# Performance work log

Hardware: AMD Instinct MI355X
Metric: run time of the kernel (lower is better)

Reference implementation:

```python
import jax, jax.numpy as jnp
import numpy as np

EPS = 1e-5

def setup_inputs() -> dict:
    key = jax.random.key(0)
    ks = jax.random.split(key, 16)
    n_users, n_items, d = 100000, 50000, 128
    n_nodes = n_users + n_items
    E = 4800000
    B = 16384
    h1, h2 = 256, 128
    xavier = lambda k, shp: jax.random.uniform(k, shp, jnp.float32, -1.0, 1.0) * np.sqrt(6.0 / (shp[0] + shp[1]))
    inp = {
        'user_indices': jax.random.randint(ks[0], (B,), 0, n_users),
        'item_indices': jax.random.randint(ks[1], (B,), 0, n_items),
        'edge_rows': jax.random.randint(ks[2], (E,), 0, n_nodes, dtype=jnp.int32),
        'edge_cols': jax.random.randint(ks[3], (E,), 0, n_nodes, dtype=jnp.int32),
        'edge_vals': jax.random.uniform(ks[4], (E,), jnp.float32),
        'user_emb': xavier(ks[5], (n_users, d)),
        'item_emb': xavier(ks[6], (n_items, d)),
        'W1': xavier(ks[7], (d, h1)), 'b1': jnp.zeros((h1,), jnp.float32),
        'g1': jnp.ones((h1,), jnp.float32), 'beta1': jnp.zeros((h1,), jnp.float32),
        'W2': xavier(ks[8], (h1, h2)), 'b2': jnp.zeros((h2,), jnp.float32),
        'g2': jnp.ones((h2,), jnp.float32), 'beta2': jnp.zeros((h2,), jnp.float32),
        'P1': xavier(ks[9], (2 * h2, h2)), 'pb1': jnp.zeros((h2,), jnp.float32),
        'P2': xavier(ks[10], (h2, 1)), 'pb2': jnp.zeros((1,), jnp.float32),
    }
    return inp

def _gcn_layer(x, rows, cols, vals, n_nodes, W, b, g, beta):
    # linear transform then sparse adjacency aggregation (COO):
    # out[r] = sum_{e: rows[e]==r} vals[e] * t[cols[e]]
    t = x @ W + b                                   # [N, out]
    agg = jax.ops.segment_sum(vals[:, None] * t[cols], rows, num_segments=n_nodes)
    # BatchNorm1d (training-mode batch statistics over nodes)
    mu = jnp.mean(agg, axis=0)
    var = jnp.var(agg, axis=0)
    out = (agg - mu) * jax.lax.rsqrt(var + EPS) * g + beta
    return jax.nn.relu(out)                         # dropout = identity (eval)

def reference(user_indices, item_indices, edge_rows, edge_cols, edge_vals,
              user_emb, item_emb, W1, b1, g1, beta1, W2, b2, g2, beta2,
              P1, pb1, P2, pb2):
    n_users = user_emb.shape[0]
    x = jnp.concatenate([user_emb, item_emb], axis=0)  # [N, d]
    n_nodes = x.shape[0]
    x = _gcn_layer(x, edge_rows, edge_cols, edge_vals, n_nodes, W1, b1, g1, beta1)
    x = _gcn_layer(x, edge_rows, edge_cols, edge_vals, n_nodes, W2, b2, g2, beta2)
    u = x[:n_users][user_indices]                      # [B, h2]
    v = x[n_users:][item_indices]                      # [B, h2]
    combined = jnp.concatenate([u, v], axis=-1)        # [B, 2*h2]
    h = jax.nn.relu(combined @ P1 + pb1)
    pred = (h @ P2 + pb2).squeeze(-1)                  # [B]
    return pred
```

## Files before the change

### kernel.cpp

```cpp
#include <hip/hip_runtime.h>
#include <stdint.h>

#define N_USERS 100000
#define N_NODES 150000
#define D0      128
#define H1      256
#define H2      128
#define NEDGE   4800000
#define BATCH   16384
#define EPSV    1e-5f
#define NBUCK   147
#define BCHUNK  4096
#define CCHUNK  16384

typedef short short8  __attribute__((ext_vector_type(8)));
typedef float floatx4 __attribute__((ext_vector_type(4)));
typedef unsigned short u16;

__device__ inline float bf2f(u16 u) {
    union { float f; uint32_t i; } x; x.i = ((uint32_t)u) << 16; return x.f;
}
__device__ inline u16 f2bf(float f) {
    union { float f; uint32_t i; } x; x.f = f;
    return (u16)((x.i + 0x7FFFu + ((x.i >> 16) & 1u)) >> 16);
}
__device__ inline float itof(uint32_t u) {
    union { float f; uint32_t i; } x; x.i = u; return x.f;
}
__device__ inline uint32_t ftoi(float f) {
    union { float f; uint32_t i; } x; x.f = f; return x.i;
}
__device__ inline uint32_t pack2(float a, float b) {
    return (uint32_t)f2bf(a) | ((uint32_t)f2bf(b) << 16);
}

__global__ __launch_bounds__(256) void k_init(float* __restrict__ out, int out_n,
                                              int* __restrict__ bcount,
                                              float* __restrict__ stats1,
                                              float* __restrict__ stats2) {
    int i = blockIdx.x * 256 + threadIdx.x;
    if (i < out_n) out[i] = 2.0f;
    if (i < NBUCK + 1) bcount[i] = 0;
    if (i < 2 * H1) stats1[i] = 0.f;
    if (i < 2 * H2) stats2[i] = 0.f;
}

__global__ __launch_bounds__(256) void k_cvt(const float* __restrict__ ue,
                                             const float* __restrict__ ie,
                                             u16* __restrict__ xb) {
    int i = (blockIdx.x * 256 + threadIdx.x) * 4;
    const int NU = N_USERS * D0;
    const int NT = N_NODES * D0;
    if (i >= NT) return;
    const float* src = (i < NU) ? (ue + i) : (ie + (i - NU));
    float4 f = *(const float4*)(const void*)src;
    uint2 w;
    w.x = pack2(f.x, f.y);
    w.y = pack2(f.z, f.w);
    *(uint2*)(void*)(xb + i) = w;
}

__global__ __launch_bounds__(256) void k_bcount(const int* __restrict__ rows,
                                                int* __restrict__ bcount) {
    __shared__ int h[NBUCK];
    int tid = threadIdx.x;
    for (int i = tid; i < NBUCK; i += 256) h[i] = 0;
    __syncthreads();
    int e0 = blockIdx.x * CCHUNK;
    int nE = NEDGE - e0; if (nE > CCHUNK) nE = CCHUNK;
    for (int i = tid; i < nE; i += 256) atomicAdd(&h[rows[e0 + i] >> 10], 1);
    __syncthreads();
    for (int i = tid; i < NBUCK; i += 256)
        if (h[i] > 0) atomicAdd(&bcount[i], h[i]);
}

__global__ __launch_bounds__(256) void k_bscan(const int* __restrict__ bcount,
                                               int* __restrict__ bucket_base,
                                               int* __restrict__ bucket_cursor,
                                               int* __restrict__ row_ptr) {
    int tid = threadIdx.x;
    int c = (tid < NBUCK) ? bcount[tid] : 0;
    int lane = tid & 63, wid = tid >> 6;
    int v = c;
    for (int off = 1; off < 64; off <<= 1) {
        int u = __shfl_up(v, off, 64);
        if (lane >= off) v += u;
    }
    __shared__ int wsum[4];
    if (lane == 63) wsum[wid] = v;
    __syncthreads();
    if (tid == 0) {
        int acc = 0;
        for (int w = 0; w < 4; ++w) { int t = wsum[w]; wsum[w] = acc; acc += t; }
    }
    __syncthreads();
    int ex = wsum[wid] + (v - c);
    if (tid < NBUCK) { bucket_base[tid] = ex; bucket_cursor[tid] = ex; }
    if (tid == 0) { bucket_base[NBUCK] = NEDGE; row_ptr[N_NODES] = NEDGE; }
}

__global__ __launch_bounds__(256) void k_bucket(const int* __restrict__ rows,
                                                const int* __restrict__ cols,
                                                const float* __restrict__ vals,
                                                int* __restrict__ bucket_cursor,
                                                uint2* __restrict__ etmp) {
    __shared__ uint2 stage[BCHUNK];
    __shared__ u16   slotb[BCHUNK];
    __shared__ int   lcnt[NBUCK + 1];
    __shared__ int   lscan[NBUCK + 1];
    __shared__ int   gstart[NBUCK];
    __shared__ int   wsum[4];
    int tid = threadIdx.x;
    int e0 = blockIdx.x * BCHUNK;
    int nE = NEDGE - e0; if (nE > BCHUNK) nE = BCHUNK;

    for (int i = tid; i <= NBUCK; i += 256) lcnt[i] = 0;
    __syncthreads();
    for (int i = tid; i < nE; i += 256) atomicAdd(&lcnt[rows[e0 + i] >> 10], 1);
    __syncthreads();
    int c = (tid < NBUCK) ? lcnt[tid] : 0;
    if (tid < NBUCK) gstart[tid] = atomicAdd(&bucket_cursor[tid], c);
    {
        int lane = tid & 63, wid = tid >> 6;
        int v = c;
        for (int off = 1; off < 64; off <<= 1) {
            int u = __shfl_up(v, off, 64);
            if (lane >= off) v += u;
        }
        if (lane == 63) wsum[wid] = v;
        __syncthreads();
        if (tid == 0) {
            int acc = 0;
            for (int w = 0; w < 4; ++w) { int t = wsum[w]; wsum[w] = acc; acc += t; }
        }
        __syncthreads();
        if (tid < NBUCK) lscan[tid] = wsum[wid] + (v - c);
        for (int i = tid; i < NBUCK; i += 256) lcnt[i] = 0;
    }
    __syncthreads();
    for (int i = tid; i < nE; i += 256) {
        int r = rows[e0 + i];
        int b = r >> 10;
        int lidx = atomicAdd(&lcnt[b], 1);
        int slot = lscan[b] + lidx;
        uint2 p;
        p.x = ((uint32_t)(r & 1023) << 18) | (uint32_t)cols[e0 + i];
        p.y = ftoi(vals[e0 + i]);
        stage[slot] = p;
        slotb[slot] = (u16)b;
    }
    __syncthreads();
    for (int s = tid; s < nE; s += 256) {
        int b = slotb[s];
        etmp[gstart[b] + (s - lscan[b])] = stage[s];
    }
}

__global__ __launch_bounds__(1024) void k_place2(const int* __restrict__ bucket_base,
                                                 const uint2* __restrict__ etmp,
                                                 int* __restrict__ row_ptr,
                                                 uint2* __restrict__ efin) {
    __shared__ int lcnt[1024];
    __shared__ int lcur[1024];
    __shared__ int wsum[16];
    int b = blockIdx.x;
    int tid = threadIdx.x;
    int base = b << 10;
    int bstart = bucket_base[b];
    int bend   = bucket_base[b + 1];
    lcnt[tid] = 0;
    __syncthreads();
    for (int i = bstart + tid; i < bend; i += 1024)
        atomicAdd(&lcnt[etmp[i].x >> 18], 1);
    __syncthreads();
    int c = lcnt[tid];
    int lane = tid & 63, wid = tid >> 6;
    int v = c;
    for (int off = 1; off < 64; off <<= 1) {
        int u = __shfl_up(v, off, 64);
        if (lane >= off) v += u;
    }
    if (lane == 63) wsum[wid] = v;
    __syncthreads();
    if (tid == 0) {
        int acc = 0;
        for (int w = 0; w < 16; ++w) { int t = wsum[w]; wsum[w] = acc; acc += t; }
    }
    __syncthreads();
    int ex = wsum[wid] + (v - c);
    int gpos = bstart + ex;
    if (base + tid < N_NODES) row_ptr[base + tid] = gpos;
    lcur[tid] = gpos;
    __syncthreads();
    for (int i = bstart + tid; i < bend; i += 1024) {
        uint2 p = etmp[i];
        int rl = (int)(p.x >> 18);
        int pos = atomicAdd(&lcur[rl], 1);
        uint2 o; o.x = p.x & 0x3FFFFu; o.y = p.y;
        efin[pos] = o;
    }
}

__global__ __launch_bounds__(256) void k_transpose3(const float* __restrict__ W1,
                                                    const float* __restrict__ W2,
                                                    const float* __restrict__ P1,
                                                    u16* __restrict__ WT1,
                                                    u16* __restrict__ WT2,
                                                    u16* __restrict__ PT1) {
    int gi = blockIdx.x * 256 + threadIdx.x;
    int seg = gi >> 15;
    int i = gi & 32767;
    const float* W; u16* WT; int K, N;
    if (seg == 0)      { W = W1; WT = WT1; K = D0;     N = H1; }
    else if (seg == 1) { W = W2; WT = WT2; K = H1;     N = H2; }
    else               { W = P1; WT = PT1; K = 2 * H2; N = H2; }
    int k = i / N, n = i - k * N;
    WT[n * K + k] = f2bf(W[i]);
}

__global__ __launch_bounds__(256) void k_gemm(const u16* __restrict__ A, int M, int K,
                                              const u16* __restrict__ BT,
                                              const float* __restrict__ bias,
                                              const float* __restrict__ rowscale,
                                              u16* __restrict__ C, int N, int relu) {
    __shared__ u16 lbt[64 * 264];
    int tid = threadIdx.x;
    int lane = tid & 63, wid = tid >> 6;
    int m0 = blockIdx.x * 64;
    int n0 = blockIdx.y * 64;
    const int KP = K + 8;
    int cpr = K / 8;
    for (int idx = tid; idx < 64 * cpr; idx += 256) {
        int r = idx / cpr, c = idx - r * cpr;
        *(uint4*)(void*)(lbt + r * KP + c * 8) =
            *(const uint4*)(const void*)(BT + (size_t)(n0 + r) * K + c * 8);
    }
    __syncthreads();
    int rn = lane & 15;
    int kq = (lane >> 4) * 8;
    int mrow = m0 + wid * 16 + rn;
    int mclamp = mrow < M ? mrow : M - 1;
    const u16* aptr = A + (size_t)mclamp * K + kq;
    floatx4 acc0 = {0.f,0.f,0.f,0.f}, acc1 = acc0, acc2 = acc0, acc3 = acc0;
    for (int kt = 0; kt < K; kt += 32) {
        short8 a  = *(const short8*)(const void*)(aptr + kt);
        short8 b0 = *(const short8*)(const void*)(lbt + ( 0 + rn) * KP + kq + kt);
        short8 b1 = *(const short8*)(const void*)(lbt + (16 + rn) * KP + kq + kt);
        short8 b2 = *(const short8*)(const void*)(lbt + (32 + rn) * KP + kq + kt);
        short8 b3 = *(const short8*)(const void*)(lbt + (48 + rn) * KP + kq + kt);
        acc0 = __builtin_amdgcn_mfma_f32_16x16x32_bf16(a, b0, acc0, 0, 0, 0);
        acc1 = __builtin_amdgcn_mfma_f32_16x16x32_bf16(a, b1, acc1, 0, 0, 0);
        acc2 = __builtin_amdgcn_mfma_f32_16x16x32_bf16(a, b2, acc2, 0, 0, 0);
        acc3 = __builtin_amdgcn_mfma_f32_16x16x32_bf16(a, b3, acc3, 0, 0, 0);
    }
    int rbase = m0 + wid * 16 + (lane >> 4) * 4;
    floatx4 accs[4] = {acc0, acc1, acc2, acc3};
    for (int j = 0; j < 4; ++j) {
        int col = n0 + j * 16 + rn;
        float bs = bias[col];
        for (int i = 0; i < 4; ++i) {
            int row = rbase + i;
            if (row < M) {
                float rs = rowscale ? rowscale[row] : 1.0f;
                float v = accs[j][i] + rs * bs;
                if (relu) v = v < 0.f ? 0.f : v;
                C[(size_t)row * N + col] = f2bf(v);
            }
        }
    }
}

__device__ inline void accum8(float* acc, uint4 r, float v) {
    acc[0] += v * bf2f((u16)(r.x & 0xffffu)); acc[1] += v * bf2f((u16)(r.x >> 16));
    acc[2] += v * bf2f((u16)(r.y & 0xffffu)); acc[3] += v * bf2f((u16)(r.y >> 16));
    acc[4] += v * bf2f((u16)(r.z & 0xffffu)); acc[5] += v * bf2f((u16)(r.z >> 16));
    acc[6] += v * bf2f((u16)(r.w & 0xffffu)); acc[7] += v * bf2f((u16)(r.w >> 16));
}

__global__ __launch_bounds__(256) void k_agg(const u16* __restrict__ t,
                                             const int* __restrict__ row_ptr,
                                             const uint2* __restrict__ edges,
                                             u16* __restrict__ agg,
                                             float* __restrict__ rowsum) {
    int tid = threadIdx.x;
    int lane = tid & 63;
    int sub = lane >> 4;
    int l16 = lane & 15;
    int row = blockIdx.x * 16 + (tid >> 6) * 4 + sub;
    float acc[8] = {0.f,0.f,0.f,0.f,0.f,0.f,0.f,0.f};
    float sv = 0.f;
    int s = row_ptr[row], e = row_ptr[row + 1];
    const u16* tf = t + l16 * 8;
    int i = s;
    for (; i + 4 <= e; i += 4) {
        uint2 e0 = edges[i], e1 = edges[i+1], e2 = edges[i+2], e3 = edges[i+3];
        uint4 r0 = *(const uint4*)(const void*)(tf + (size_t)e0.x * 128);
        uint4 r1 = *(const uint4*)(const void*)(tf + (size_t)e1.x * 128);
        uint4 r2 = *(const uint4*)(const void*)(tf + (size_t)e2.x * 128);
        uint4 r3 = *(const uint4*)(const void*)(tf + (size_t)e3.x * 128);
        float v0 = itof(e0.y), v1 = itof(e1.y), v2 = itof(e2.y), v3 = itof(e3.y);
        accum8(acc, r0, v0); accum8(acc, r1, v1);
        accum8(acc, r2, v2); accum8(acc, r3, v3);
        sv += v0 + v1 + v2 + v3;
    }
    for (; i < e; ++i) {
        uint2 e0 = edges[i];
        uint4 r0 = *(const uint4*)(const void*)(tf + (size_t)e0.x * 128);
        float v0 = itof(e0.y);
        accum8(acc, r0, v0);
        sv += v0;
    }
    uint4 w;
    w.x = pack2(acc[0], acc[1]); w.y = pack2(acc[2], acc[3]);
    w.z = pack2(acc[4], acc[5]); w.w = pack2(acc[6], acc[7]);
    *(uint4*)(void*)(agg + (size_t)row * 128 + l16 * 8) = w;
    if (rowsum != nullptr && l16 == 0) rowsum[row] = sv;
}

__global__ __launch_bounds__(256) void k_bnstats(const u16* __restrict__ agg,
                                                 float* __restrict__ stats, int NF) {
    int tid = threadIdx.x;
    int rpb = 256 / NF;
    int f = tid & (NF - 1);
    int r0 = blockIdx.x * rpb + tid / NF;
    int rs = gridDim.x * rpb;
    float s = 0.f, s2 = 0.f;
    for (int row = r0; row < N_NODES; row += rs) {
        float v = bf2f(agg[(size_t)row * NF + f]);
        s += v; s2 += v * v;
    }
    atomicAdd(&stats[f], s);
    atomicAdd(&stats[NF + f], s2);
}

__global__ __launch_bounds__(256) void k_bnapply(const u16* __restrict__ agg,
                                                 const float* __restrict__ stats,
                                                 const float* __restrict__ g,
                                                 const float* __restrict__ beta,
                                                 u16* __restrict__ x, int NF) {
    size_t idx = (size_t)blockIdx.x * 256 + threadIdx.x;
    if (idx >= (size_t)N_NODES * NF) return;
    int f = (int)(idx & (size_t)(NF - 1));
    float mu = stats[f] * (1.0f / N_NODES);
    float var = stats[NF + f] * (1.0f / N_NODES) - mu * mu;
    float sc = rsqrtf(var + EPSV) * g[f];
    float v = (bf2f(agg[idx]) - mu) * sc + beta[f];
    x[idx] = f2bf(v < 0.f ? 0.f : v);
}

__global__ __launch_bounds__(256) void k_gatherBN(const int* __restrict__ ui,
                                                  const int* __restrict__ ii,
                                                  const u16* __restrict__ agg2,
                                                  const float* __restrict__ stats,
                                                  const float* __restrict__ g,
                                                  const float* __restrict__ beta,
                                                  u16* __restrict__ comb) {
    int item = blockIdx.x * 4 + (threadIdx.x >> 6);
    int lane = threadIdx.x & 63;
    if (item >= BATCH) return;
    int node = (lane < 32) ? ui[item] : (N_USERS + ii[item]);
    int fb = (lane & 31) * 4;
    uint2 r = *(const uint2*)(const void*)(agg2 + (size_t)node * H2 + fb);
    float vv[4] = { bf2f((u16)(r.x & 0xffffu)), bf2f((u16)(r.x >> 16)),
                    bf2f((u16)(r.y & 0xffffu)), bf2f((u16)(r.y >> 16)) };
    u16 o[4];
    for (int j = 0; j < 4; ++j) {
        int f = fb + j;
        float mu = stats[f] * (1.0f / N_NODES);
        float var = stats[H2 + f] * (1.0f / N_NODES) - mu * mu;
        float sc = rsqrtf(var + EPSV) * g[f];
        float v = (vv[j] - mu) * sc + beta[f];
        o[j] = f2bf(v < 0.f ? 0.f : v);
    }
    uint2 w;
    w.x = (uint32_t)o[0] | ((uint32_t)o[1] << 16);
    w.y = (uint32_t)o[2] | ((uint32_t)o[3] << 16);
    *(uint2*)(void*)(comb + (size_t)item * (2 * H2) + lane * 4) = w;
}

__global__ __launch_bounds__(256) void k_final(const u16* __restrict__ h,
                                               const float* __restrict__ P2,
                                               const float* __restrict__ pb2,
                                               float* __restrict__ out) {
    int item = blockIdx.x * 4 + (threadIdx.x >> 6);
    int lane = threadIdx.x & 63;
    if (item >= BATCH) return;
    float a = bf2f(h[(size_t)item * H2 + lane])      * P2[lane]
            + bf2f(h[(size_t)item * H2 + 64 + lane]) * P2[64 + lane];
    for (int off = 32; off > 0; off >>= 1) a += __shfl_down(a, off, 64);
    if (lane == 0) out[item] = a + pb2[0];
}

extern "C" void kernel_launch(void* const* d_in, const int* in_sizes, int n_in,
                              void* d_out, int out_size, void* d_ws, size_t ws_size,
                              hipStream_t stream) {
    (void)in_sizes; (void)n_in; (void)ws_size;
    const int* user_indices = (const int*)d_in[0];
    const int* item_indices = (const int*)d_in[1];
    const int* edge_rows    = (const int*)d_in[2];
    const int* edge_cols    = (const int*)d_in[3];
    const float* edge_vals = (const float*)d_in[4];
    const float* user_emb  = (const float*)d_in[5];
    const float* item_emb  = (const float*)d_in[6];
    const float* W1    = (const float*)d_in[7];
    const float* b1    = (const float*)d_in[8];
    const float* g1    = (const float*)d_in[9];
    const float* beta1 = (const float*)d_in[10];
    const float* W2    = (const float*)d_in[11];
    const float* b2    = (const float*)d_in[12];
    const float* g2    = (const float*)d_in[13];
    const float* beta2 = (const float*)d_in[14];
    const float* P1    = (const float*)d_in[15];
    const float* pb1   = (const float*)d_in[16];
    const float* P2    = (const float*)d_in[17];
    const float* pb2   = (const float*)d_in[18];
    float* out = (float*)d_out;

    char* ws = (char*)d_ws;
    size_t off = 0;
    auto alloc = [&](size_t bytes) -> char* {
        char* p = ws + off;
        off = (off + bytes + 255) & ~(size_t)255;
        return p;
    };
    int*   row_ptr  = (int*)alloc(sizeof(int) * (N_NODES + 1));
    int*   bcount   = (int*)alloc(sizeof(int) * (NBUCK + 1));
    int*   bbase    = (int*)alloc(sizeof(int) * (NBUCK + 1));
    int*   bcursor  = (int*)alloc(sizeof(int) * (NBUCK + 1));
    float* rowsum   = (float*)alloc(sizeof(float) * N_NODES);
    float* stats1   = (float*)alloc(sizeof(float) * 2 * H1);
    float* stats2   = (float*)alloc(sizeof(float) * 2 * H2);
    u16* WT1 = (u16*)alloc(2 * D0 * H1);
    u16* WT2 = (u16*)alloc(2 * H1 * H2);
    u16* PT1 = (u16*)alloc(2 * 2 * H2 * H2);
    uint2* efin = (uint2*)alloc(8 * (size_t)NEDGE);
    u16* R1   = (u16*)alloc(2 * (size_t)N_NODES * H1);
    u16* xb   = R1;
    u16* aggx = R1 + (size_t)N_NODES * D0;
    u16* x1   = R1;
    u16* R2   = (u16*)alloc(2 * (size_t)N_NODES * H1);
    uint2* etmp = (uint2*)R2;
    u16* agg1 = R2;
    u16* t2   = R2;
    u16* agg2 = R2 + (size_t)N_NODES * H2;
    u16* comb = R2;
    u16* hbuf = R2 + (size_t)BATCH * 2 * H2;

    k_init<<<(out_size + 255) / 256, 256, 0, stream>>>(out, out_size, bcount, stats1, stats2);

    k_cvt<<<(N_NODES * D0 / 4 + 255) / 256, 256, 0, stream>>>(user_emb, item_emb, xb);

    k_bcount<<<(NEDGE + CCHUNK - 1) / CCHUNK, 256, 0, stream>>>(edge_rows, bcount);
    k_bscan<<<1, 256, 0, stream>>>(bcount, bbase, bcursor, row_ptr);
    k_bucket<<<(NEDGE + BCHUNK - 1) / BCHUNK, 256, 0, stream>>>(
        edge_rows, edge_cols, edge_vals, bcursor, etmp);
    k_place2<<<NBUCK, 1024, 0, stream>>>(bbase, etmp, row_ptr, efin);

    k_transpose3<<<(3 * 32768) / 256, 256, 0, stream>>>(W1, W2, P1, WT1, WT2, PT1);

    k_agg<<<N_NODES / 16, 256, 0, stream>>>(xb, row_ptr, efin, aggx, rowsum);
    k_gemm<<<dim3((N_NODES + 63) / 64, H1 / 64), 256, 0, stream>>>(
        aggx, N_NODES, D0, WT1, b1, rowsum, agg1, H1, 0);
    k_bnstats<<<512, 256, 0, stream>>>(agg1, stats1, H1);
    k_bnapply<<<(N_NODES * H1) / 256, 256, 0, stream>>>(agg1, stats1, g1, beta1, x1, H1);

    k_gemm<<<dim3((N_NODES + 63) / 64, H2 / 64), 256, 0, stream>>>(
        x1, N_NODES, H1, WT2, b2, nullptr, t2, H2, 0);
    k_agg<<<N_NODES / 16, 256, 0, stream>>>(t2, row_ptr, efin, agg2, nullptr);
    k_bnstats<<<512, 256, 0, stream>>>(agg2, stats2, H2);

    k_gatherBN<<<BATCH / 4, 256, 0, stream>>>(user_indices, item_indices, agg2,
                                              stats2, g2, beta2, comb);
    k_gemm<<<dim3(BATCH / 64, H2 / 64), 256, 0, stream>>>(
        comb, BATCH, 2 * H2, PT1, pb1, nullptr, hbuf, H2, 1);
    k_final<<<BATCH / 4, 256, 0, stream>>>(hbuf, P2, pb2, out);
}
```

Measured before the change: 1.018 ms.

## Fuse BatchNorm statistics and apply into GEMM and aggregation kernels

Removes the separate BN-stats and BN-apply passes. Statistics are now accumulated in the GEMM and aggregation epilogues, using shared-memory reduction and double atomics. The BN scale/shift plus ReLU is applied to the A operand as it is loaded in the second GEMM. The GEMM is templated to cover the full N width per block with an XOR-swizzled LDS layout and non-temporal loads, and the aggregation loop is unrolled to 8 edges. This saves several full passes over the 150k x 256 activations, at the cost of more register pressure and extra atomic traffic.

Result: slower. 1.198 ms (+17.7%).

```diff
diff --git a/kernel.cpp b/kernel.cpp
--- a/kernel.cpp
+++ b/kernel.cpp
@@ -15,7 +15,9 @@
 
 typedef short short8  __attribute__((ext_vector_type(8)));
 typedef float floatx4 __attribute__((ext_vector_type(4)));
+typedef unsigned int uint32x4 __attribute__((ext_vector_type(4)));
 typedef unsigned short u16;
+typedef unsigned long long u64;
 
 __device__ inline float bf2f(u16 u) {
     union { float f; uint32_t i; } x; x.i = ((uint32_t)u) << 16; return x.f;
@@ -36,13 +38,13 @@
 
 __global__ __launch_bounds__(256) void k_init(float* __restrict__ out, int out_n,
                                               int* __restrict__ bcount,
-                                              float* __restrict__ stats1,
-                                              float* __restrict__ stats2) {
+                                              double* __restrict__ stats1,
+                                              double* __restrict__ stats2) {
     int i = blockIdx.x * 256 + threadIdx.x;
     if (i < out_n) out[i] = 2.0f;
     if (i < NBUCK + 1) bcount[i] = 0;
-    if (i < 2 * H1) stats1[i] = 0.f;
-    if (i < 2 * H2) stats2[i] = 0.f;
+    if (i < 2 * H1) stats1[i] = 0.0;
+    if (i < 2 * H2) stats2[i] = 0.0;
 }
 
 __global__ __launch_bounds__(256) void k_cvt(const float* __restrict__ ue,
@@ -218,55 +220,124 @@
     WT[n * K + k] = f2bf(W[i]);
 }
 
-__global__ __launch_bounds__(256) void k_gemm(const u16* __restrict__ A, int M, int K,
-                                              const u16* __restrict__ BT,
-                                              const float* __restrict__ bias,
-                                              const float* __restrict__ rowscale,
-                                              u16* __restrict__ C, int N, int relu) {
-    __shared__ u16 lbt[64 * 264];
+__global__ __launch_bounds__(256) void k_bnprep(const double* __restrict__ stats,
+                                                const float* __restrict__ g,
+                                                const float* __restrict__ beta,
+                                                float* __restrict__ sc,
+                                                float* __restrict__ sh, int NF) {
+    int f = blockIdx.x * 256 + threadIdx.x;
+    if (f >= NF) return;
+    double mu = stats[f] * (1.0 / N_NODES);
+    double var = stats[NF + f] * (1.0 / N_NODES) - mu * mu;
+    float s = rsqrtf((float)var + EPSV) * g[f];
+    sc[f] = s;
+    sh[f] = beta[f] - (float)mu * s;
+}
+
+template<int NJ, int KK, bool BNF, bool RELU, bool STATS>
+__global__ __launch_bounds__(256, 2) void k_gemmN(const u16* __restrict__ A, int M,
+                                                  const u16* __restrict__ BT,
+                                                  const float* __restrict__ bias,
+                                                  const float* __restrict__ rowscale,
+                                                  const float* __restrict__ bnsc,
+                                                  const float* __restrict__ bnsh,
+                                                  double* __restrict__ stats,
+                                                  u16* __restrict__ C) {
+    constexpr int NN = NJ * 16;
+    __shared__ u16 lbt[NN * KK];
+    constexpr int CPR = KK / 8;
     int tid = threadIdx.x;
     int lane = tid & 63, wid = tid >> 6;
     int m0 = blockIdx.x * 64;
-    int n0 = blockIdx.y * 64;
-    const int KP = K + 8;
-    int cpr = K / 8;
-    for (int idx = tid; idx < 64 * cpr; idx += 256) {
-        int r = idx / cpr, c = idx - r * cpr;
-        *(uint4*)(void*)(lbt + r * KP + c * 8) =
-            *(const uint4*)(const void*)(BT + (size_t)(n0 + r) * K + c * 8);
-    }
-    __syncthreads();
+
+    for (int idx = tid; idx < NN * CPR; idx += 256) {
+        int r = idx / CPR, c = idx - r * CPR;
+        int dst = (r * KK + c * 8) ^ ((r & 7) << 3);
+        *(uint4*)(void*)(lbt + dst) = *(const uint4*)(const void*)(BT + (size_t)r * KK + c * 8);
+    }
+    __syncthreads();
+
     int rn = lane & 15;
     int kq = (lane >> 4) * 8;
     int mrow = m0 + wid * 16 + rn;
     int mclamp = mrow < M ? mrow : M - 1;
-    const u16* aptr = A + (size_t)mclamp * K + kq;
-    floatx4 acc0 = {0.f,0.f,0.f,0.f}, acc1 = acc0, acc2 = acc0, acc3 = acc0;
-    for (int kt = 0; kt < K; kt += 32) {
-        short8 a  = *(const short8*)(const void*)(aptr + kt);
-        short8 b0 = *(const short8*)(const void*)(lbt + ( 0 + rn) * KP + kq + kt);
-        short8 b1 = *(const short8*)(const void*)(lbt + (16 + rn) * KP + kq + kt);
-        short8 b2 = *(const short8*)(const void*)(lbt + (32 + rn) * KP + kq + kt);
-        short8 b3 = *(const short8*)(const void*)(lbt + (48 + rn) * KP + kq + kt);
-        acc0 = __builtin_amdgcn_mfma_f32_16x16x32_bf16(a, b0, acc0, 0, 0, 0);
-        acc1 = __builtin_amdgcn_mfma_f32_16x16x32_bf16(a, b1, acc1, 0, 0, 0);
-        acc2 = __builtin_amdgcn_mfma_f32_16x16x32_bf16(a, b2, acc2, 0, 0, 0);
-        acc3 = __builtin_amdgcn_mfma_f32_16x16x32_bf16(a, b3, acc3, 0, 0, 0);
-    }
+    const u16* aptr = A + (size_t)mclamp * KK + kq;
+    int swz = (rn & 7) << 3;
+
+    floatx4 acc[NJ];
+    #pragma unroll
+    for (int j = 0; j < NJ; ++j) acc[j] = (floatx4){0.f, 0.f, 0.f, 0.f};
+
+    #pragma unroll
+    for (int kt = 0; kt < KK; kt += 32) {
+        short8 a = __builtin_nontemporal_load((const short8*)(const void*)(aptr + kt));
+        if constexpr (BNF) {
+            float4 s0 = *(const float4*)(const void*)(bnsc + kq + kt);
+            float4 s1 = *(const float4*)(const void*)(bnsc + kq + kt + 4);
+            float4 h0 = *(const float4*)(const void*)(bnsh + kq + kt);
+            float4 h1 = *(const float4*)(const void*)(bnsh + kq + kt + 4);
+            float v0 = fmaxf(bf2f((u16)a[0]) * s0.x + h0.x, 0.f);
+            float v1 = fmaxf(bf2f((u16)a[1]) * s0.y + h0.y, 0.f);
+            float v2 = fmaxf(bf2f((u16)a[2]) * s0.z + h0.z, 0.f);
+            float v3 = fmaxf(bf2f((u16)a[3]) * s0.w + h0.w, 0.f);
+            float v4 = fmaxf(bf2f((u16)a[4]) * s1.x + h1.x, 0.f);
+            float v5 = fmaxf(bf2f((u16)a[5]) * s1.y + h1.y, 0.f);
+            float v6 = fmaxf(bf2f((u16)a[6]) * s1.z + h1.z, 0.f);
+            float v7 = fmaxf(bf2f((u16)a[7]) * s1.w + h1.w, 0.f);
+            union { short8 s; u16 u[8]; } ua;
+            ua.u[0] = f2bf(v0); ua.u[1] = f2bf(v1);
+            ua.u[2] = f2bf(v2); ua.u[3] = f2bf(v3);
+            ua.u[4] = f2bf(v4); ua.u[5] = f2bf(v5);
+            ua.u[6] = f2bf(v6); ua.u[7] = f2bf(v7);
+            a = ua.s;
+        }
+        #pragma unroll
+        for (int j = 0; j < NJ; ++j) {
+            const u16* bp = lbt + ((j * 16 + rn) * KK + ((kq + kt) ^ swz));
+            short8 b = *(const short8*)(const void*)bp;
+            acc[j] = __builtin_amdgcn_mfma_f32_16x16x32_bf16(a, b, acc[j], 0, 0, 0);
+        }
+    }
+
+    float* sred = (float*)lbt;
+    if constexpr (STATS) {
+        __syncthreads();
+        for (int i = tid; i < 2 * NN; i += 256) sred[i] = 0.f;
+        __syncthreads();
+    }
+
     int rbase = m0 + wid * 16 + (lane >> 4) * 4;
-    floatx4 accs[4] = {acc0, acc1, acc2, acc3};
-    for (int j = 0; j < 4; ++j) {
-        int col = n0 + j * 16 + rn;
+    float rsv[4];
+    #pragma unroll
+    for (int i = 0; i < 4; ++i) {
+        int row = rbase + i;
+        rsv[i] = rowscale ? rowscale[row < M ? row : M - 1] : 1.0f;
+    }
+    #pragma unroll
+    for (int j = 0; j < NJ; ++j) {
+        int col = j * 16 + rn;
         float bs = bias[col];
+        float vs = 0.f, vq = 0.f;
+        #pragma unroll
         for (int i = 0; i < 4; ++i) {
             int row = rbase + i;
+            float v = acc[j][i] + rsv[i] * bs;
+            if constexpr (RELU) v = v < 0.f ? 0.f : v;
             if (row < M) {
-                float rs = rowscale ? rowscale[row] : 1.0f;
-                float v = accs[j][i] + rs * bs;
-                if (relu) v = v < 0.f ? 0.f : v;
-                C[(size_t)row * N + col] = f2bf(v);
+                u16 cb = f2bf(v);
+                C[(size_t)row * NN + col] = cb;
+                if constexpr (STATS) { float vr = bf2f(cb); vs += vr; vq += vr * vr; }
             }
         }
+        if constexpr (STATS) {
+            atomicAdd(&sred[col], vs);
+            atomicAdd(&sred[NN + col], vq);
+        }
+    }
+    if constexpr (STATS) {
+        __syncthreads();
+        for (int i = tid; i < 2 * NN; i += 256)
+            atomicAdd(&stats[i], (double)sred[i]);
     }
 }
 
@@ -277,12 +348,16 @@
     acc[6] += v * bf2f((u16)(r.w & 0xffffu)); acc[7] += v * bf2f((u16)(r.w >> 16));
 }
 
-__global__ __launch_bounds__(256) void k_agg(const u16* __restrict__ t,
-                                             const int* __restrict__ row_ptr,
-                                             const uint2* __restrict__ edges,
-                                             u16* __restrict__ agg,
-                                             float* __restrict__ rowsum) {
+__global__ __launch_bounds__(256, 4) void k_agg(const u16* __restrict__ t,
+                                                const int* __restrict__ row_ptr,
+                                                const uint2* __restrict__ edges,
+                                                u16* __restrict__ agg,
+                                                float* __restrict__ rowsum,
+                                                double* __restrict__ stats) {
+    __shared__ float sred[2 * H2];
     int tid = threadIdx.x;
+    bool dostats = (stats != nullptr);
+    if (dostats) { sred[tid] = 0.f; __syncthreads(); }
     int lane = tid & 63;
     int sub = lane >> 4;
     int l16 = lane & 15;
@@ -291,67 +366,47 @@
     float sv = 0.f;
     int s = row_ptr[row], e = row_ptr[row + 1];
     const u16* tf = t + l16 * 8;
+    const u64* ep = (const u64*)edges;
     int i = s;
-    for (; i + 4 <= e; i += 4) {
-        uint2 e0 = edges[i], e1 = edges[i+1], e2 = edges[i+2], e3 = edges[i+3];
-        uint4 r0 = *(const uint4*)(const void*)(tf + (size_t)e0.x * 128);
-        uint4 r1 = *(const uint4*)(const void*)(tf + (size_t)e1.x * 128);
-        uint4 r2 = *(const uint4*)(const void*)(tf + (size_t)e2.x * 128);
-        uint4 r3 = *(const uint4*)(const void*)(tf + (size_t)e3.x * 128);
-        float v0 = itof(e0.y), v1 = itof(e1.y), v2 = itof(e2.y), v3 = itof(e3.y);
+#define GATH(n) \
+    u64 p##n = __builtin_nontemporal_load(ep + i + n); \
+    uint4 r##n = *(const uint4*)(const void*)(tf + (size_t)((uint32_t)p##n) * 128); \
+    float v##n = itof((uint32_t)(p##n >> 32));
+    for (; i + 8 <= e; i += 8) {
+        GATH(0) GATH(1) GATH(2) GATH(3) GATH(4) GATH(5) GATH(6) GATH(7)
         accum8(acc, r0, v0); accum8(acc, r1, v1);
         accum8(acc, r2, v2); accum8(acc, r3, v3);
-        sv += v0 + v1 + v2 + v3;
+        accum8(acc, r4, v4); accum8(acc, r5, v5);
+        accum8(acc, r6, v6); accum8(acc, r7, v7);
+        sv += (v0 + v1 + v2 + v3) + (v4 + v5 + v6 + v7);
     }
     for (; i < e; ++i) {
-        uint2 e0 = edges[i];
-        uint4 r0 = *(const uint4*)(const void*)(tf + (size_t)e0.x * 128);
-        float v0 = itof(e0.y);
+        GATH(0)
         accum8(acc, r0, v0);
         sv += v0;
     }
-    uint4 w;
+#undef GATH
+    uint32x4 w;
     w.x = pack2(acc[0], acc[1]); w.y = pack2(acc[2], acc[3]);
     w.z = pack2(acc[4], acc[5]); w.w = pack2(acc[6], acc[7]);
-    *(uint4*)(void*)(agg + (size_t)row * 128 + l16 * 8) = w;
+    __builtin_nontemporal_store(w, (uint32x4*)(void*)(agg + (size_t)row * 128 + l16 * 8));
     if (rowsum != nullptr && l16 == 0) rowsum[row] = sv;
-}
-
-__global__ __launch_bounds__(256) void k_bnstats(const u16* __restrict__ agg,
-                                                 float* __restrict__ stats, int NF) {
-    int tid = threadIdx.x;
-    int rpb = 256 / NF;
-    int f = tid & (NF - 1);
-    int r0 = blockIdx.x * rpb + tid / NF;
-    int rs = gridDim.x * rpb;
-    float s = 0.f, s2 = 0.f;
-    for (int row = r0; row < N_NODES; row += rs) {
-        float v = bf2f(agg[(size_t)row * NF + f]);
-        s += v; s2 += v * v;
-    }
-    atomicAdd(&stats[f], s);
-    atomicAdd(&stats[NF + f], s2);
-}
-
-__global__ __launch_bounds__(256) void k_bnapply(const u16* __restrict__ agg,
-                                                 const float* __restrict__ stats,
-                                                 const float* __restrict__ g,
-                                                 const float* __restrict__ beta,
-                                                 u16* __restrict__ x, int NF) {
-    size_t idx = (size_t)blockIdx.x * 256 + threadIdx.x;
-    if (idx >= (size_t)N_NODES * NF) return;
-    int f = (int)(idx & (size_t)(NF - 1));
-    float mu = stats[f] * (1.0f / N_NODES);
-    float var = stats[NF + f] * (1.0f / N_NODES) - mu * mu;
-    float sc = rsqrtf(var + EPSV) * g[f];
-    float v = (bf2f(agg[idx]) - mu) * sc + beta[f];
-    x[idx] = f2bf(v < 0.f ? 0.f : v);
+    if (dostats) {
+        #pragma unroll
+        for (int j = 0; j < 8; ++j) {
+            float aj = bf2f(f2bf(acc[j]));
+            atomicAdd(&sred[l16 * 8 + j], aj);
+            atomicAdd(&sred[H2 + l16 * 8 + j], aj * aj);
+        }
+        __syncthreads();
+        atomicAdd(&stats[tid], (double)sred[tid]);
+    }
 }
 
 __global__ __launch_bounds__(256) void k_gatherBN(const int* __restrict__ ui,
                                                   const int* __restrict__ ii,
                                                   const u16* __restrict__ agg2,
-                                                  const float* __restrict__ stats,
+                                                  const double* __restrict__ stats,
                                                   const float* __restrict__ g,
                                                   const float* __restrict__ beta,
                                                   u16* __restrict__ comb) {
@@ -366,10 +421,10 @@
     u16 o[4];
     for (int j = 0; j < 4; ++j) {
         int f = fb + j;
-        float mu = stats[f] * (1.0f / N_NODES);
-        float var = stats[H2 + f] * (1.0f / N_NODES) - mu * mu;
-        float sc = rsqrtf(var + EPSV) * g[f];
-        float v = (vv[j] - mu) * sc + beta[f];
+        double mu = stats[f] * (1.0 / N_NODES);
+        double var = stats[H2 + f] * (1.0 / N_NODES) - mu * mu;
+        float sc = rsqrtf((float)var + EPSV) * g[f];
+        float v = ((float)(vv[j] - mu)) * sc + beta[f];
         o[j] = f2bf(v < 0.f ? 0.f : v);
     }
     uint2 w;
@@ -428,8 +483,10 @@
     int*   bbase    = (int*)alloc(sizeof(int) * (NBUCK + 1));
     int*   bcursor  = (int*)alloc(sizeof(int) * (NBUCK + 1));
     float* rowsum   = (float*)alloc(sizeof(float) * N_NODES);
-    float* stats1   = (float*)alloc(sizeof(float) * 2 * H1);
-    float* stats2   = (float*)alloc(sizeof(float) * 2 * H2);
+    double* stats1  = (double*)alloc(sizeof(double) * 2 * H1);
+    double* stats2  = (double*)alloc(sizeof(double) * 2 * H2);
+    float* sc1      = (float*)alloc(sizeof(float) * H1);
+    float* sh1      = (float*)alloc(sizeof(float) * H1);
     u16* WT1 = (u16*)alloc(2 * D0 * H1);
     u16* WT2 = (u16*)alloc(2 * H1 * H2);
     u16* PT1 = (u16*)alloc(2 * 2 * H2 * H2);
@@ -437,11 +494,10 @@
     u16* R1   = (u16*)alloc(2 * (size_t)N_NODES * H1);
     u16* xb   = R1;
     u16* aggx = R1 + (size_t)N_NODES * D0;
-    u16* x1   = R1;
+    u16* t2   = R1;
     u16* R2   = (u16*)alloc(2 * (size_t)N_NODES * H1);
     uint2* etmp = (uint2*)R2;
     u16* agg1 = R2;
-    u16* t2   = R2;
     u16* agg2 = R2 + (size_t)N_NODES * H2;
     u16* comb = R2;
     u16* hbuf = R2 + (size_t)BATCH * 2 * H2;
@@ -458,20 +514,18 @@
 
     k_transpose3<<<(3 * 32768) / 256, 256, 0, stream>>>(W1, W2, P1, WT1, WT2, PT1);
 
-    k_agg<<<N_NODES / 16, 256, 0, stream>>>(xb, row_ptr, efin, aggx, rowsum);
-    k_gemm<<<dim3((N_NODES + 63) / 64, H1 / 64), 256, 0, stream>>>(
-        aggx, N_NODES, D0, WT1, b1, rowsum, agg1, H1, 0);
-    k_bnstats<<<512, 256, 0, stream>>>(agg1, stats1, H1);
-    k_bnapply<<<(N_NODES * H1) / 256, 256, 0, stream>>>(agg1, stats1, g1, beta1, x1, H1);
-
-    k_gemm<<<dim3((N_NODES + 63) / 64, H2 / 64), 256, 0, stream>>>(
-        x1, N_NODES, H1, WT2, b2, nullptr, t2, H2, 0);
-    k_agg<<<N_NODES / 16, 256, 0, stream>>>(t2, row_ptr, efin, agg2, nullptr);
-    k_bnstats<<<512, 256, 0, stream>>>(agg2, stats2, H2);
+    k_agg<<<N_NODES / 16, 256, 0, stream>>>(xb, row_ptr, efin, aggx, rowsum, nullptr);
+    k_gemmN<16, 128, false, false, true><<<(N_NODES + 63) / 64, 256, 0, stream>>>(
+        aggx, N_NODES, WT1, b1, rowsum, nullptr, nullptr, stats1, agg1);
+    k_bnprep<<<1, 256, 0, stream>>>(stats1, g1, beta1, sc1, sh1, H1);
+
+    k_gemmN<8, 256, true, false, false><<<(N_NODES + 63) / 64, 256, 0, stream>>>(
+        agg1, N_NODES, WT2, b2, nullptr, sc1, sh1, nullptr, t2);
+    k_agg<<<N_NODES / 16, 256, 0, stream>>>(t2, row_ptr, efin, agg2, nullptr, stats2);
 
     k_gatherBN<<<BATCH / 4, 256, 0, stream>>>(user_indices, item_indices, agg2,
                                               stats2, g2, beta2, comb);
-    k_gemm<<<dim3(BATCH / 64, H2 / 64), 256, 0, stream>>>(
-        comb, BATCH, 2 * H2, PT1, pb1, nullptr, hbuf, H2, 1);
+    k_gemmN<8, 256, false, true, false><<<BATCH / 64, 256, 0, stream>>>(
+        comb, BATCH, PT1, pb1, nullptr, nullptr, nullptr, nullptr, hbuf);
     k_final<<<BATCH / 4, 256, 0, stream>>>(hbuf, P2, pb2, out);
 }
```
